# Performance work log

Hardware: AMD Instinct MI355X
Metric: run time of the kernel (lower is better)

The kernel has to match this reference:

```python
import jax, jax.numpy as jnp
import numpy as np
import math

H = 1024  # hidden_size
BELOW = 1024
ABOVE = 1024
B = 2048  # batch


def setup_inputs() -> dict:
    key = jax.random.key(0)
    ks = jax.random.split(key, 10)
    stdv = 1.0 / math.sqrt(H)
    W_hh = jax.random.uniform(ks[0], (4 * H + 1, BELOW), minval=-stdv, maxval=stdv, dtype=jnp.float32)
    U_11 = jax.random.uniform(ks[1], (4 * H + 1, H), minval=-stdv, maxval=stdv, dtype=jnp.float32)
    U_21 = jax.random.uniform(ks[2], (4 * H + 1, ABOVE), minval=-stdv, maxval=stdv, dtype=jnp.float32)
    bias = jax.random.uniform(ks[3], (4 * H + 1,), minval=-stdv, maxval=stdv, dtype=jnp.float32)
    bias = bias.at[-1].set(2.0 / math.sqrt(H))  # reset_parameters sets last bias entry
    c = jax.random.normal(ks[4], (H, B), dtype=jnp.float32)
    h_bottom = jax.random.normal(ks[5], (BELOW, B), dtype=jnp.float32)
    h = jax.random.normal(ks[6], (H, B), dtype=jnp.float32)
    h_top = jax.random.normal(ks[7], (ABOVE, B), dtype=jnp.float32)
    z = jax.random.bernoulli(ks[8], 0.5, (1, B)).astype(jnp.float32)
    z_bottom = jax.random.bernoulli(ks[9], 0.5, (1, B)).astype(jnp.float32)
    return {"c": c, "h_bottom": h_bottom, "h": h, "h_top": h_top, "z": z,
            "z_bottom": z_bottom, "W_hh": W_hh, "U_11": U_11, "U_21": U_21, "bias": bias}


def hard_sigmoid(x, slope=1.0):
    return jnp.clip((x * slope + 1.0) / 2.0, 0.0, 1.0)


def binary_threshold_ste(z_hat, threshold=0.5):
    hard = (z_hat > threshold).astype(z_hat.dtype)
    # straight-through: forward hard, backward identity
    return z_hat + jax.lax.stop_gradient(hard - z_hat)


def reference(c, h_bottom, h, h_top, z, z_bottom, W_hh, U_11, U_21, bias):
    a = 1.0
    s_recur = W_hh @ h_bottom                 # (4H+1, B)
    s_topdown = z * (U_21 @ h_top)            # (4H+1, B)
    s_bottomup = z * (U_11 @ h)               # (4H+1, B)
    f_slice = s_recur + s_topdown + s_bottomup + bias[:, None]
    forgetgate = f_slice[0 * H:1 * H]
    ingate = f_slice[1 * H:2 * H]
    outgate = f_slice[2 * H:3 * H]
    cellgate = f_slice[3 * H:4 * H]
    z_gate = f_slice[4 * H:4 * H + 1]         # (1, B)
    f = jax.nn.sigmoid(forgetgate)
    i = jax.nn.sigmoid(ingate)
    o = jax.nn.sigmoid(outgate)
    g = jnp.tanh(cellgate)
    z_hat = hard_sigmoid(z_gate, slope=a)
    one = 1.0
    c_new = z * (i * g) + (one - z) * (one - z_bottom) * c + (one - z) * z_bottom * (f * c + i * g)
    tanh_c = jnp.tanh(c_new)
    h_new = z * o * tanh_c + (one - z) * (one - z_bottom) * h + (one - z) * z_bottom * o * tanh_c
    z_new = binary_threshold_ste(z_hat)
    return (h_new, c_new, z_new)
```

## Files before the change

### kernel.cpp

```cpp
#include <hip/hip_runtime.h>
#include <hip/hip_bf16.h>

#define HB_ELEMS ((size_t)1024 * 2048)
#define P_ELEMS  ((size_t)4096 * 2048)

typedef __bf16 bfx8 __attribute__((ext_vector_type(8)));
typedef float f32x4 __attribute__((ext_vector_type(4)));

__device__ __forceinline__ float b2f(unsigned short u) {
    union { unsigned int i; float f; } v; v.i = ((unsigned int)u) << 16; return v.f;
}
__device__ __forceinline__ unsigned short f2b(float f) {
    __hip_bfloat16 h = __float2bfloat16(f);
    return *reinterpret_cast<unsigned short*>(&h);
}
__device__ __forceinline__ float loadf(const void* p, size_t i, bool f32) {
    return f32 ? ((const float*)p)[i] : b2f(((const unsigned short*)p)[i]);
}
__device__ __forceinline__ float sigf(float x) { return 1.0f / (1.0f + __expf(-x)); }

__device__ __forceinline__ void cell_math(float fp, float ip, float op, float gp,
                                           float cc, float hh, float zc, float zv,
                                           float& hn, float& cn) {
    float f = sigf(fp), i = sigf(ip), o = sigf(op), g = tanhf(gp);
    float ig = i * g;
    cn = zc * ig + (1.0f - zc) * (1.0f - zv) * cc + (1.0f - zc) * zv * (f * cc + ig);
    float tc = tanhf(cn);
    hn = zc * o * tc + (1.0f - zc) * (1.0f - zv) * hh + (1.0f - zc) * zv * o * tc;
}

__global__ void detect_k(const unsigned short* __restrict__ w, int* __restrict__ flag) {
    int lane = threadIdx.x;
    bool hit = false;
    #pragma unroll
    for (int i = 0; i < 4; ++i) {
        unsigned e = (w[lane + i * 64] >> 7) & 0xFF;
        hit |= (e >= 126);
    }
    unsigned long long m = __ballot(hit);
    if (lane == 0) *flag = (m != 0ULL) ? 1 : 0;
}

__global__ __launch_bounds__(256) void build_bt(
    const void* __restrict__ hb, const void* __restrict__ h,
    const void* __restrict__ ht, const void* __restrict__ z,
    unsigned short* __restrict__ BT, const int* __restrict__ flagp)
{
    const bool f32 = (*flagp != 0);
    int tid = blockIdx.x * 256 + threadIdx.x;
    int b   = tid & 2047;
    int kg8 = tid >> 11;
    int k   = kg8 * 8;

    const void* src; int kl; bool sc;
    if (k < 1024)      { src = hb; kl = k;        sc = false; }
    else if (k < 2048) { src = h;  kl = k - 1024; sc = true;  }
    else               { src = ht; kl = k - 2048; sc = true;  }

    bool zero = sc && (loadf(z, b, f32) == 0.0f);
    unsigned short t[8];
    if (zero) {
        #pragma unroll
        for (int j = 0; j < 8; ++j) t[j] = 0;
    } else if (f32) {
        #pragma unroll
        for (int j = 0; j < 8; ++j) t[j] = f2b(((const float*)src)[(size_t)(kl + j) * 2048 + b]);
    } else {
        #pragma unroll
        for (int j = 0; j < 8; ++j) t[j] = ((const unsigned short*)src)[(size_t)(kl + j) * 2048 + b];
    }
    uint4 v;
    v.x = (unsigned)t[0] | ((unsigned)t[1] << 16);
    v.y = (unsigned)t[2] | ((unsigned)t[3] << 16);
    v.z = (unsigned)t[4] | ((unsigned)t[5] << 16);
    v.w = (unsigned)t[6] | ((unsigned)t[7] << 16);
    *reinterpret_cast<uint4*>(&BT[(size_t)b * 3072 + k]) = v;
}

__global__ __launch_bounds__(256, 2) void gemm_split(
    const void* __restrict__ Whh, const void* __restrict__ U11, const void* __restrict__ U21,
    const unsigned short* __restrict__ BT,
    unsigned short* __restrict__ P, const int* __restrict__ flagp)
{
    const bool f32 = (*flagp != 0);
    __shared__ __align__(16) unsigned short As[2][128 * 64];
    __shared__ __align__(16) unsigned short Bs[2][128 * 64];

    int id  = (blockIdx.z * 32 + blockIdx.y) * 16 + blockIdx.x;
    int sid = (id & 7) * 192 + (id >> 3);
    const int n0   = (sid & 15) * 128;
    const int j0   = ((sid >> 4) & 31) * 32;
    const int kseg = sid >> 9;
    const void* Asrc = (kseg == 0) ? Whh : ((kseg == 1) ? U11 : U21);
    const int kbase = kseg * 1024;

    const int wave = threadIdx.x >> 6;
    const int lane = threadIdx.x & 63;
    const int srow = wave * 8 + (lane >> 3);
    const int scol_sw = (((lane & 7) ^ (lane >> 3)) * 8);
    const int wm = wave >> 1, wn = wave & 1;
    const int lr = lane & 15, kg = lane >> 4;
    const int lr7 = lr & 7;

    f32x4 acc[4][4] = {};

    auto stage = [&](int buf, int k0) {
        #pragma unroll
        for (int r = 0; r < 4; ++r) {
            const unsigned short* g = &BT[(size_t)(n0 + r * 32 + srow) * 3072 + kbase + k0 + scol_sw];
            __builtin_amdgcn_global_load_lds(
                (const __attribute__((address_space(1))) void*)g,
                (__attribute__((address_space(3))) void*)((char*)&Bs[buf][0] + r * 4096 + wave * 1024),
                16, 0, 0);
        }
        if (!f32) {
            #pragma unroll
            for (int r = 0; r < 4; ++r) {
                const unsigned short* g = (const unsigned short*)Asrc
                    + (size_t)(r * 1024 + j0 + srow) * 1024 + k0 + scol_sw;
                __builtin_amdgcn_global_load_lds(
                    (const __attribute__((address_space(1))) void*)g,
                    (__attribute__((address_space(3))) void*)((char*)&As[buf][0] + r * 4096 + wave * 1024),
                    16, 0, 0);
            }
        } else {
            #pragma unroll
            for (int r = 0; r < 4; ++r) {
                int trow = r * 32 + srow;
                int dst  = trow * 64 + scol_sw;
                const float* g = (const float*)Asrc + (size_t)(r * 1024 + j0 + srow) * 1024
                               + k0 + (lane & 7) * 8;
                float4 a0 = *reinterpret_cast<const float4*>(g);
                float4 a1 = *reinterpret_cast<const float4*>(g + 4);
                uint4 v;
                v.x = (unsigned)f2b(a0.x) | ((unsigned)f2b(a0.y) << 16);
                v.y = (unsigned)f2b(a0.z) | ((unsigned)f2b(a0.w) << 16);
                v.z = (unsigned)f2b(a1.x) | ((unsigned)f2b(a1.y) << 16);
                v.w = (unsigned)f2b(a1.z) | ((unsigned)f2b(a1.w) << 16);
                *reinterpret_cast<uint4*>(&As[buf][dst]) = v;
            }
        }
    };

    stage(0, 0);

    #pragma unroll 2
    for (int t = 0; t < 16; ++t) {
        const int cur = t & 1;
        if (t < 15) stage(cur ^ 1, (t + 1) * 64);

        if (f32) {
            asm volatile("s_waitcnt vmcnt(0) lgkmcnt(0)" ::: "memory");
        } else if (t < 15) {
            asm volatile("s_waitcnt vmcnt(8)" ::: "memory");
        } else {
            asm volatile("s_waitcnt vmcnt(0)" ::: "memory");
        }
        __builtin_amdgcn_sched_barrier(0);
        __builtin_amdgcn_s_barrier();
        __builtin_amdgcn_sched_barrier(0);

        #pragma unroll
        for (int kk = 0; kk < 64; kk += 32) {
            const int c0 = kk >> 3;
            const int csw = ((c0 + kg) ^ lr7) * 8;
            bfx8 av[4], bv[4];
            #pragma unroll
            for (int mi = 0; mi < 4; ++mi)
                av[mi] = *reinterpret_cast<const bfx8*>(
                    &As[cur][(wm * 64 + mi * 16 + lr) * 64 + csw]);
            #pragma unroll
            for (int ni = 0; ni < 4; ++ni)
                bv[ni] = *reinterpret_cast<const bfx8*>(
                    &Bs[cur][(wn * 64 + ni * 16 + lr) * 64 + csw]);
            #pragma unroll
            for (int mi = 0; mi < 4; ++mi)
                #pragma unroll
                for (int ni = 0; ni < 4; ++ni)
                    acc[mi][ni] = __builtin_amdgcn_mfma_f32_16x16x32_bf16(av[mi], bv[ni], acc[mi][ni], 0, 0, 0);
        }

        __builtin_amdgcn_sched_barrier(0);
        __builtin_amdgcn_s_barrier();
        __builtin_amdgcn_sched_barrier(0);
    }

    unsigned short* Pp = P + (size_t)kseg * P_ELEMS;
    #pragma unroll
    for (int mi = 0; mi < 4; ++mi) {
        #pragma unroll
        for (int ni = 0; ni < 4; ++ni) {
            int col = n0 + wn * 64 + ni * 16 + lr;
            #pragma unroll
            for (int r = 0; r < 4; ++r) {
                int trow = wm * 64 + mi * 16 + kg * 4 + r;
                int gate = trow >> 5, jj = trow & 31;
                size_t m = (size_t)gate * 1024 + j0 + jj;
                Pp[m * 2048 + col] = f2b(acc[mi][ni][r]);
            }
        }
    }
}

__global__ __launch_bounds__(256) void epilogue_split(
    const unsigned short* __restrict__ P, const void* __restrict__ c_,
    const void* __restrict__ h_, const void* __restrict__ z_,
    const void* __restrict__ zb_, const void* __restrict__ bias_,
    void* __restrict__ out_, const int* __restrict__ flagp)
{
    const bool f32 = (*flagp != 0);
    int tid = blockIdx.x * 256 + threadIdx.x;
    int j = tid >> 9;
    int b = (tid & 511) << 2;
    const size_t jb = (size_t)j * 2048 + b;

    float pre[4][4];
    #pragma unroll
    for (int g = 0; g < 4; ++g) {
        size_t row = (size_t)(g * 1024 + j) * 2048 + b;
        ushort4 s0 = *reinterpret_cast<const ushort4*>(&P[row]);
        ushort4 s1 = *reinterpret_cast<const ushort4*>(&P[P_ELEMS + row]);
        ushort4 s2 = *reinterpret_cast<const ushort4*>(&P[2 * P_ELEMS + row]);
        float bv = loadf(bias_, g * 1024 + j, f32);
        pre[g][0] = b2f(s0.x) + b2f(s1.x) + b2f(s2.x) + bv;
        pre[g][1] = b2f(s0.y) + b2f(s1.y) + b2f(s2.y) + bv;
        pre[g][2] = b2f(s0.z) + b2f(s1.z) + b2f(s2.z) + bv;
        pre[g][3] = b2f(s0.w) + b2f(s1.w) + b2f(s2.w) + bv;
    }

    float hn[4], cn[4];
    #pragma unroll
    for (int e = 0; e < 4; ++e) {
        float zc = loadf(z_, b + e, f32);
        float zv = loadf(zb_, b + e, f32);
        float cc = loadf(c_, jb + e, f32);
        float hh = loadf(h_, jb + e, f32);
        cell_math(pre[0][e], pre[1][e], pre[2][e], pre[3][e], cc, hh, zc, zv, hn[e], cn[e]);
    }
    if (f32) {
        float4 ho = {hn[0], hn[1], hn[2], hn[3]};
        float4 co = {cn[0], cn[1], cn[2], cn[3]};
        *reinterpret_cast<float4*>(&((float*)out_)[jb]) = ho;
        *reinterpret_cast<float4*>(&((float*)out_)[HB_ELEMS + jb]) = co;
    } else {
        ushort4 ho = {f2b(hn[0]), f2b(hn[1]), f2b(hn[2]), f2b(hn[3])};
        ushort4 co = {f2b(cn[0]), f2b(cn[1]), f2b(cn[2]), f2b(cn[3])};
        *reinterpret_cast<ushort4*>(&((unsigned short*)out_)[jb]) = ho;
        *reinterpret_cast<ushort4*>(&((unsigned short*)out_)[HB_ELEMS + jb]) = co;
    }
}

__global__ __launch_bounds__(256) void gemm_fused(
    const void* __restrict__ Whh, const void* __restrict__ U11, const void* __restrict__ U21,
    const unsigned short* __restrict__ BT,
    const void* __restrict__ c_, const void* __restrict__ h_,
    const void* __restrict__ z_, const void* __restrict__ zb_,
    const void* __restrict__ bias_, void* __restrict__ out_,
    const int* __restrict__ flagp)
{
    const bool f32 = (*flagp != 0);
    __shared__ __align__(16) unsigned short As[128 * 64];
    __shared__ __align__(16) unsigned short Bs[128 * 64];

    const int n0 = blockIdx.x * 128;
    const int j0 = blockIdx.y * 32;
    const int wave = threadIdx.x >> 6;
    const int lane = threadIdx.x & 63;
    const int srow = wave * 8 + (lane >> 3);
    const int scol = (lane & 7) * 8;
    const int lr = lane & 15, kg = lane >> 4;

    f32x4 acc[8][2] = {};

    for (int k0 = 0; k0 < 3072; k0 += 64) {
        int seg = k0 >> 10, kl = k0 & 1023;
        const void* Asrc = (seg == 0) ? Whh : ((seg == 1) ? U11 : U21);

        __syncthreads();
        #pragma unroll
        for (int r = 0; r < 4; ++r) {
            const unsigned short* g = &BT[(size_t)(n0 + r * 32 + srow) * 3072 + k0 + scol];
            __builtin_amdgcn_global_load_lds(
                (const __attribute__((address_space(1))) void*)g,
                (__attribute__((address_space(3))) void*)((char*)Bs + r * 4096 + wave * 1024),
                16, 0, 0);
        }
        if (!f32) {
            #pragma unroll
            for (int r = 0; r < 4; ++r) {
                const unsigned short* g = (const unsigned short*)Asrc
                    + (size_t)(r * 1024 + j0 + srow) * 1024 + kl + scol;
                __builtin_amdgcn_global_load_lds(
                    (const __attribute__((address_space(1))) void*)g,
                    (__attribute__((address_space(3))) void*)((char*)As + r * 4096 + wave * 1024),
                    16, 0, 0);
            }
        } else {
            #pragma unroll
            for (int r = 0; r < 4; ++r) {
                int trow = r * 32 + srow;
                const float* g = (const float*)Asrc + (size_t)(r * 1024 + j0 + srow) * 1024 + kl + scol;
                float4 a0 = *reinterpret_cast<const float4*>(g);
                float4 a1 = *reinterpret_cast<const float4*>(g + 4);
                uint4 v;
                v.x = (unsigned)f2b(a0.x) | ((unsigned)f2b(a0.y) << 16);
                v.y = (unsigned)f2b(a0.z) | ((unsigned)f2b(a0.w) << 16);
                v.z = (unsigned)f2b(a1.x) | ((unsigned)f2b(a1.y) << 16);
                v.w = (unsigned)f2b(a1.z) | ((unsigned)f2b(a1.w) << 16);
                *reinterpret_cast<uint4*>(&As[trow * 64 + scol]) = v;
            }
        }
        __syncthreads();

        #pragma unroll
        for (int kk = 0; kk < 64; kk += 32) {
            bfx8 bv0 = *reinterpret_cast<const bfx8*>(&Bs[(wave * 32 + lr) * 64 + kk + kg * 8]);
            bfx8 bv1 = *reinterpret_cast<const bfx8*>(&Bs[(wave * 32 + 16 + lr) * 64 + kk + kg * 8]);
            #pragma unroll
            for (int mi = 0; mi < 8; ++mi) {
                bfx8 af = *reinterpret_cast<const bfx8*>(&As[(mi * 16 + lr) * 64 + kk + kg * 8]);
                acc[mi][0] = __builtin_amdgcn_mfma_f32_16x16x32_bf16(af, bv0, acc[mi][0], 0, 0, 0);
                acc[mi][1] = __builtin_amdgcn_mfma_f32_16x16x32_bf16(af, bv1, acc[mi][1], 0, 0, 0);
            }
        }
    }

    #pragma unroll
    for (int ni = 0; ni < 2; ++ni) {
        int b = n0 + wave * 32 + ni * 16 + lr;
        float zc = loadf(z_, b, f32);
        float zv = loadf(zb_, b, f32);
        #pragma unroll
        for (int mh = 0; mh < 2; ++mh) {
            #pragma unroll
            for (int r = 0; r < 4; ++r) {
                int j = j0 + mh * 16 + kg * 4 + r;
                float fp = acc[0 + mh][ni][r] + loadf(bias_, j, f32);
                float ip = acc[2 + mh][ni][r] + loadf(bias_, 1024 + j, f32);
                float op = acc[4 + mh][ni][r] + loadf(bias_, 2048 + j, f32);
                float gp = acc[6 + mh][ni][r] + loadf(bias_, 3072 + j, f32);
                float cc = loadf(c_, (size_t)j * 2048 + b, f32);
                float hh = loadf(h_, (size_t)j * 2048 + b, f32);
                float hn, cn;
                cell_math(fp, ip, op, gp, cc, hh, zc, zv, hn, cn);
                if (f32) {
                    ((float*)out_)[(size_t)j * 2048 + b] = hn;
                    ((float*)out_)[HB_ELEMS + (size_t)j * 2048 + b] = cn;
                } else {
                    ((unsigned short*)out_)[(size_t)j * 2048 + b] = f2b(hn);
                    ((unsigned short*)out_)[HB_ELEMS + (size_t)j * 2048 + b] = f2b(cn);
                }
            }
        }
    }
}

__global__ __launch_bounds__(256) void zrow_part(
    const void* __restrict__ Whh, const void* __restrict__ U11, const void* __restrict__ U21,
    const void* __restrict__ hb, const void* __restrict__ h, const void* __restrict__ ht,
    float* __restrict__ pz, const int* __restrict__ flagp)
{
    const bool f32 = (*flagp != 0);
    const int c   = blockIdx.x;
    const int mat = c >> 5;
    const int k0  = (c & 31) * 32;
    const int b0  = threadIdx.x * 8;

    const void* W = (mat == 0) ? Whh : ((mat == 1) ? U11 : U21);
    const void* X = (mat == 0) ? hb  : ((mat == 1) ? h   : ht);
    const size_t wrow = (size_t)4096 * 1024;

    float acc[8] = {0.f, 0.f, 0.f, 0.f, 0.f, 0.f, 0.f, 0.f};
    if (!f32) {
        const unsigned short* Wp = (const unsigned short*)W;
        const unsigned short* Xp = (const unsigned short*)X;
        #pragma unroll 4
        for (int kk = 0; kk < 32; ++kk) {
            int k = k0 + kk;
            float w = b2f(Wp[wrow + k]);
            ushort4 xa = *reinterpret_cast<const ushort4*>(&Xp[(size_t)k * 2048 + b0]);
            ushort4 xb = *reinterpret_cast<const ushort4*>(&Xp[(size_t)k * 2048 + b0 + 4]);
            acc[0] += w * b2f(xa.x); acc[1] += w * b2f(xa.y);
            acc[2] += w * b2f(xa.z); acc[3] += w * b2f(xa.w);
            acc[4] += w * b2f(xb.x); acc[5] += w * b2f(xb.y);
            acc[6] += w * b2f(xb.z); acc[7] += w * b2f(xb.w);
        }
    } else {
        const float* Wp = (const float*)W;
        const float* Xp = (const float*)X;
        #pragma unroll 4
        for (int kk = 0; kk < 32; ++kk) {
            int k = k0 + kk;
            float w = Wp[wrow + k];
            float4 xa = *reinterpret_cast<const float4*>(&Xp[(size_t)k * 2048 + b0]);
            float4 xb = *reinterpret_cast<const float4*>(&Xp[(size_t)k * 2048 + b0 + 4]);
            acc[0] += w * xa.x; acc[1] += w * xa.y; acc[2] += w * xa.z; acc[3] += w * xa.w;
            acc[4] += w * xb.x; acc[5] += w * xb.y; acc[6] += w * xb.z; acc[7] += w * xb.w;
        }
    }
    #pragma unroll
    for (int j = 0; j < 8; ++j)
        pz[(size_t)c * 2048 + b0 + j] = acc[j];
}

__global__ __launch_bounds__(256) void zrow_reduce(
    const float* __restrict__ pz, const void* __restrict__ z_,
    const void* __restrict__ bias_, void* __restrict__ out_,
    const int* __restrict__ flagp)
{
    const bool f32 = (*flagp != 0);
    int b = blockIdx.x * 256 + threadIdx.x;
    float a1 = 0.f, a2 = 0.f, a3 = 0.f;
    #pragma unroll
    for (int c = 0; c < 32; ++c)  a1 += pz[(size_t)c * 2048 + b];
    #pragma unroll
    for (int c = 32; c < 64; ++c) a2 += pz[(size_t)c * 2048 + b];
    #pragma unroll
    for (int c = 64; c < 96; ++c) a3 += pz[(size_t)c * 2048 + b];
    float zc = loadf(z_, b, f32);
    float s = a1 + zc * (a2 + a3) + loadf(bias_, 4096, f32);
    float zh = (s + 1.0f) * 0.5f;
    zh = fminf(fmaxf(zh, 0.0f), 1.0f);
    float zn = (zh > 0.5f) ? 1.0f : 0.0f;
    if (f32) ((float*)out_)[2 * HB_ELEMS + b] = zn;
    else     ((unsigned short*)out_)[2 * HB_ELEMS + b] = f2b(zn);
}

__global__ __launch_bounds__(256) void zrow_k(
    const void* __restrict__ Whh, const void* __restrict__ U11, const void* __restrict__ U21,
    const void* __restrict__ hb, const void* __restrict__ h, const void* __restrict__ ht,
    const void* __restrict__ z_, const void* __restrict__ bias_,
    void* __restrict__ out_, const int* __restrict__ flagp)
{
    const bool f32 = (*flagp != 0);
    int b = blockIdx.x * 256 + threadIdx.x;
    float a1 = 0.f, a2 = 0.f, a3 = 0.f;
    const size_t wrow = (size_t)4096 * 1024;
    for (int k = 0; k < 1024; ++k) {
        a1 += loadf(Whh, wrow + k, f32) * loadf(hb, (size_t)k * 2048 + b, f32);
        a2 += loadf(U11, wrow + k, f32) * loadf(h,  (size_t)k * 2048 + b, f32);
        a3 += loadf(U21, wrow + k, f32) * loadf(ht, (size_t)k * 2048 + b, f32);
    }
    float zc = loadf(z_, b, f32);
    float s = a1 + zc * (a2 + a3) + loadf(bias_, 4096, f32);
    float zh = (s + 1.0f) * 0.5f;
    zh = fminf(fmaxf(zh, 0.0f), 1.0f);
    float zn = (zh > 0.5f) ? 1.0f : 0.0f;
    if (f32) ((float*)out_)[2 * HB_ELEMS + b] = zn;
    else     ((unsigned short*)out_)[2 * HB_ELEMS + b] = f2b(zn);
}

__global__ __launch_bounds__(256) void fallback_k(
    const void* __restrict__ Whh, const void* __restrict__ U11, const void* __restrict__ U21,
    const void* __restrict__ hb, const void* __restrict__ h, const void* __restrict__ ht,
    const void* __restrict__ c_, const void* __restrict__ z_, const void* __restrict__ zb_,
    const void* __restrict__ bias_, void* __restrict__ out_, const int* __restrict__ flagp)
{
    const bool f32 = (*flagp != 0);
    int b = blockIdx.x * 256 + threadIdx.x;
    int j = blockIdx.y;
    float zc = loadf(z_, b, f32);
    float a[4] = {0.f, 0.f, 0.f, 0.f};
    for (int k = 0; k < 1024; ++k) {
        float xb = loadf(hb, (size_t)k * 2048 + b, f32);
        #pragma unroll
        for (int g = 0; g < 4; ++g)
            a[g] += loadf(Whh, (size_t)(g * 1024 + j) * 1024 + k, f32) * xb;
    }
    for (int k = 0; k < 1024; ++k) {
        float xh = zc * loadf(h, (size_t)k * 2048 + b, f32);
        #pragma unroll
        for (int g = 0; g < 4; ++g)
            a[g] += loadf(U11, (size_t)(g * 1024 + j) * 1024 + k, f32) * xh;
    }
    for (int k = 0; k < 1024; ++k) {
        float xt = zc * loadf(ht, (size_t)k * 2048 + b, f32);
        #pragma unroll
        for (int g = 0; g < 4; ++g)
            a[g] += loadf(U21, (size_t)(g * 1024 + j) * 1024 + k, f32) * xt;
    }
    float fp = a[0] + loadf(bias_, j, f32);
    float ip = a[1] + loadf(bias_, 1024 + j, f32);
    float op = a[2] + loadf(bias_, 2048 + j, f32);
    float gp = a[3] + loadf(bias_, 3072 + j, f32);
    float cc = loadf(c_, (size_t)j * 2048 + b, f32);
    float hh = loadf(h,  (size_t)j * 2048 + b, f32);
    float zv = loadf(zb_, b, f32);
    float hn, cn;
    cell_math(fp, ip, op, gp, cc, hh, zc, zv, hn, cn);
    if (f32) {
        ((float*)out_)[(size_t)j * 2048 + b] = hn;
        ((float*)out_)[HB_ELEMS + (size_t)j * 2048 + b] = cn;
    } else {
        ((unsigned short*)out_)[(size_t)j * 2048 + b] = f2b(hn);
        ((unsigned short*)out_)[HB_ELEMS + (size_t)j * 2048 + b] = f2b(cn);
    }
}

extern "C" void kernel_launch(void* const* d_in, const int* in_sizes, int n_in,
                              void* d_out, int out_size, void* d_ws, size_t ws_size,
                              hipStream_t stream)
{
    const void* c    = d_in[0];
    const void* hb   = d_in[1];
    const void* h    = d_in[2];
    const void* ht   = d_in[3];
    const void* z    = d_in[4];
    const void* zb   = d_in[5];
    const void* Whh  = d_in[6];
    const void* U11  = d_in[7];
    const void* U21  = d_in[8];
    const void* bias = d_in[9];

    int* flag = (int*)d_ws;
    unsigned short* BT = (unsigned short*)((char*)d_ws + 4096);
    const size_t bt_bytes = (size_t)2048 * 3072 * 2;
    float* pz = (float*)((char*)d_ws + 4096 + bt_bytes);
    const size_t pz_bytes = (size_t)96 * 2048 * 4;
    unsigned short* P = (unsigned short*)((char*)d_ws + 4096 + bt_bytes + pz_bytes);
    const size_t p_bytes = 3 * P_ELEMS * 2;

    const size_t need_bt    = 4096 + bt_bytes;
    const size_t need_pz    = need_bt + pz_bytes;
    const size_t need_split = need_pz + p_bytes;

    if (ws_size < 4) return;

    detect_k<<<1, 64, 0, stream>>>((const unsigned short*)Whh, flag);

    if (ws_size >= need_split) {
        build_bt<<<(2048 * 384) / 256, 256, 0, stream>>>(hb, h, ht, z, BT, flag);
        gemm_split<<<dim3(16, 32, 3), 256, 0, stream>>>(Whh, U11, U21, BT, P, flag);
        epilogue_split<<<(1024 * 512) / 256, 256, 0, stream>>>(P, c, h, z, zb, bias, d_out, flag);
    } else if (ws_size >= need_bt) {
        build_bt<<<(2048 * 384) / 256, 256, 0, stream>>>(hb, h, ht, z, BT, flag);
        gemm_fused<<<dim3(16, 32), 256, 0, stream>>>(Whh, U11, U21, BT,
                                                     c, h, z, zb, bias, d_out, flag);
    } else {
        fallback_k<<<dim3(8, 1024), 256, 0, stream>>>(Whh, U11, U21, hb, h, ht,
                                                      c, z, zb, bias, d_out, flag);
    }

    if (ws_size >= need_pz) {
        zrow_part<<<96, 256, 0, stream>>>(Whh, U11, U21, hb, h, ht, pz, flag);
        zrow_reduce<<<8, 256, 0, stream>>>(pz, z, bias, d_out, flag);
    } else {
        zrow_k<<<8, 256, 0, stream>>>(Whh, U11, U21, hb, h, ht, z, bias, d_out, flag);
    }
}
```

Baseline: 135.1 us.

## Enlarge GEMM tiles to 256x256 with 512 threads and split K in two

The split GEMM now uses 256x256 output tiles with 8 waves per block, each wave holding an 8x4 MFMA accumulator grid. K is split into two halves of 1536 that cross weight-matrix boundaries, replacing the three per-matrix segments. This halves the partial-sum buffer and removes one partial read in the epilogue, and the larger tiles reuse each loaded operand more. The trade-offs are 64 KB of LDS per block, more accumulator registers, and only 256 blocks, which may leave CUs underused.

```diff
diff --git a/kernel.cpp b/kernel.cpp
--- a/kernel.cpp
+++ b/kernel.cpp
@@ -77,59 +77,62 @@
     *reinterpret_cast<uint4*>(&BT[(size_t)b * 3072 + k]) = v;
 }
 
-__global__ __launch_bounds__(256, 2) void gemm_split(
+__global__ __launch_bounds__(512, 2) void gemm_split(
     const void* __restrict__ Whh, const void* __restrict__ U11, const void* __restrict__ U21,
     const unsigned short* __restrict__ BT,
     unsigned short* __restrict__ P, const int* __restrict__ flagp)
 {
     const bool f32 = (*flagp != 0);
-    __shared__ __align__(16) unsigned short As[2][128 * 64];
-    __shared__ __align__(16) unsigned short Bs[2][128 * 64];
-
-    int id  = (blockIdx.z * 32 + blockIdx.y) * 16 + blockIdx.x;
-    int sid = (id & 7) * 192 + (id >> 3);
-    const int n0   = (sid & 15) * 128;
-    const int j0   = ((sid >> 4) & 31) * 32;
-    const int kseg = sid >> 9;
-    const void* Asrc = (kseg == 0) ? Whh : ((kseg == 1) ? U11 : U21);
-    const int kbase = kseg * 1024;
+    __shared__ __align__(16) unsigned short As[2][256 * 64];
+    __shared__ __align__(16) unsigned short Bs[2][256 * 64];
+
+    int id  = (blockIdx.z * 16 + blockIdx.y) * 8 + blockIdx.x;
+    int sid = (id & 7) * 32 + (id >> 3);
+    const int n0   = (sid & 7) * 256;
+    const int j0   = ((sid >> 3) & 15) * 64;
+    const int kseg = sid >> 7;
+    const int kbase = kseg * 1536;
 
     const int wave = threadIdx.x >> 6;
     const int lane = threadIdx.x & 63;
-    const int srow = wave * 8 + (lane >> 3);
     const int scol_sw = (((lane & 7) ^ (lane >> 3)) * 8);
-    const int wm = wave >> 1, wn = wave & 1;
+    const int wm = wave >> 2, wn = wave & 3;
     const int lr = lane & 15, kg = lane >> 4;
     const int lr7 = lr & 7;
 
-    f32x4 acc[4][4] = {};
-
-    auto stage = [&](int buf, int k0) {
+    f32x4 acc[8][4] = {};
+
+    auto stage = [&](int buf, int kt) {
+        const int kglob = kbase + kt * 64;
+        const int seg = kglob >> 10, kl = kglob & 1023;
+        const void* Ap = (seg == 0) ? Whh : ((seg == 1) ? U11 : U21);
+
         #pragma unroll
         for (int r = 0; r < 4; ++r) {
-            const unsigned short* g = &BT[(size_t)(n0 + r * 32 + srow) * 3072 + kbase + k0 + scol_sw];
+            int trow = r * 64 + wave * 8 + (lane >> 3);
+            const unsigned short* g = &BT[(size_t)(n0 + trow) * 3072 + kglob + scol_sw];
             __builtin_amdgcn_global_load_lds(
                 (const __attribute__((address_space(1))) void*)g,
-                (__attribute__((address_space(3))) void*)((char*)&Bs[buf][0] + r * 4096 + wave * 1024),
+                (__attribute__((address_space(3))) void*)((char*)&Bs[buf][0] + r * 8192 + wave * 1024),
                 16, 0, 0);
         }
         if (!f32) {
             #pragma unroll
             for (int r = 0; r < 4; ++r) {
-                const unsigned short* g = (const unsigned short*)Asrc
-                    + (size_t)(r * 1024 + j0 + srow) * 1024 + k0 + scol_sw;
+                int trow = r * 64 + wave * 8 + (lane >> 3);
+                size_t arow = (size_t)((trow >> 6) * 1024 + j0 + (trow & 63));
+                const unsigned short* g = (const unsigned short*)Ap + arow * 1024 + kl + scol_sw;
                 __builtin_amdgcn_global_load_lds(
                     (const __attribute__((address_space(1))) void*)g,
-                    (__attribute__((address_space(3))) void*)((char*)&As[buf][0] + r * 4096 + wave * 1024),
+                    (__attribute__((address_space(3))) void*)((char*)&As[buf][0] + r * 8192 + wave * 1024),
                     16, 0, 0);
             }
         } else {
             #pragma unroll
             for (int r = 0; r < 4; ++r) {
-                int trow = r * 32 + srow;
-                int dst  = trow * 64 + scol_sw;
-                const float* g = (const float*)Asrc + (size_t)(r * 1024 + j0 + srow) * 1024
-                               + k0 + (lane & 7) * 8;
+                int trow = r * 64 + wave * 8 + (lane >> 3);
+                size_t arow = (size_t)((trow >> 6) * 1024 + j0 + (trow & 63));
+                const float* g = (const float*)Ap + arow * 1024 + kl + (lane & 7) * 8;
                 float4 a0 = *reinterpret_cast<const float4*>(g);
                 float4 a1 = *reinterpret_cast<const float4*>(g + 4);
                 uint4 v;
@@ -137,7 +140,7 @@
                 v.y = (unsigned)f2b(a0.z) | ((unsigned)f2b(a0.w) << 16);
                 v.z = (unsigned)f2b(a1.x) | ((unsigned)f2b(a1.y) << 16);
                 v.w = (unsigned)f2b(a1.z) | ((unsigned)f2b(a1.w) << 16);
-                *reinterpret_cast<uint4*>(&As[buf][dst]) = v;
+                *reinterpret_cast<uint4*>(&As[buf][trow * 64 + scol_sw]) = v;
             }
         }
     };
@@ -145,13 +148,13 @@
     stage(0, 0);
 
     #pragma unroll 2
-    for (int t = 0; t < 16; ++t) {
-        const int cur = t & 1;
-        if (t < 15) stage(cur ^ 1, (t + 1) * 64);
+    for (int kt = 0; kt < 24; ++kt) {
+        const int cur = kt & 1;
+        if (kt < 23) stage(cur ^ 1, kt + 1);
 
         if (f32) {
             asm volatile("s_waitcnt vmcnt(0) lgkmcnt(0)" ::: "memory");
-        } else if (t < 15) {
+        } else if (kt < 23) {
             asm volatile("s_waitcnt vmcnt(8)" ::: "memory");
         } else {
             asm volatile("s_waitcnt vmcnt(0)" ::: "memory");
@@ -161,20 +164,19 @@
         __builtin_amdgcn_sched_barrier(0);
 
         #pragma unroll
-        for (int kk = 0; kk < 64; kk += 32) {
-            const int c0 = kk >> 3;
-            const int csw = ((c0 + kg) ^ lr7) * 8;
-            bfx8 av[4], bv[4];
-            #pragma unroll
-            for (int mi = 0; mi < 4; ++mi)
+        for (int kk = 0; kk < 2; ++kk) {
+            const int csw = ((kk * 4 + kg) ^ lr7) * 8;
+            bfx8 av[8], bv[4];
+            #pragma unroll
+            for (int mi = 0; mi < 8; ++mi)
                 av[mi] = *reinterpret_cast<const bfx8*>(
-                    &As[cur][(wm * 64 + mi * 16 + lr) * 64 + csw]);
+                    &As[cur][(wm * 128 + mi * 16 + lr) * 64 + csw]);
             #pragma unroll
             for (int ni = 0; ni < 4; ++ni)
                 bv[ni] = *reinterpret_cast<const bfx8*>(
                     &Bs[cur][(wn * 64 + ni * 16 + lr) * 64 + csw]);
             #pragma unroll
-            for (int mi = 0; mi < 4; ++mi)
+            for (int mi = 0; mi < 8; ++mi)
                 #pragma unroll
                 for (int ni = 0; ni < 4; ++ni)
                     acc[mi][ni] = __builtin_amdgcn_mfma_f32_16x16x32_bf16(av[mi], bv[ni], acc[mi][ni], 0, 0, 0);
@@ -187,14 +189,14 @@
 
     unsigned short* Pp = P + (size_t)kseg * P_ELEMS;
     #pragma unroll
-    for (int mi = 0; mi < 4; ++mi) {
+    for (int mi = 0; mi < 8; ++mi) {
         #pragma unroll
         for (int ni = 0; ni < 4; ++ni) {
             int col = n0 + wn * 64 + ni * 16 + lr;
             #pragma unroll
             for (int r = 0; r < 4; ++r) {
-                int trow = wm * 64 + mi * 16 + kg * 4 + r;
-                int gate = trow >> 5, jj = trow & 31;
+                int trow = wm * 128 + mi * 16 + kg * 4 + r;
+                int gate = trow >> 6, jj = trow & 63;
                 size_t m = (size_t)gate * 1024 + j0 + jj;
                 Pp[m * 2048 + col] = f2b(acc[mi][ni][r]);
             }
@@ -220,12 +222,11 @@
         size_t row = (size_t)(g * 1024 + j) * 2048 + b;
         ushort4 s0 = *reinterpret_cast<const ushort4*>(&P[row]);
         ushort4 s1 = *reinterpret_cast<const ushort4*>(&P[P_ELEMS + row]);
-        ushort4 s2 = *reinterpret_cast<const ushort4*>(&P[2 * P_ELEMS + row]);
         float bv = loadf(bias_, g * 1024 + j, f32);
-        pre[g][0] = b2f(s0.x) + b2f(s1.x) + b2f(s2.x) + bv;
-        pre[g][1] = b2f(s0.y) + b2f(s1.y) + b2f(s2.y) + bv;
-        pre[g][2] = b2f(s0.z) + b2f(s1.z) + b2f(s2.z) + bv;
-        pre[g][3] = b2f(s0.w) + b2f(s1.w) + b2f(s2.w) + bv;
+        pre[g][0] = b2f(s0.x) + b2f(s1.x) + bv;
+        pre[g][1] = b2f(s0.y) + b2f(s1.y) + bv;
+        pre[g][2] = b2f(s0.z) + b2f(s1.z) + bv;
+        pre[g][3] = b2f(s0.w) + b2f(s1.w) + bv;
     }
 
     float hn[4], cn[4];
@@ -518,7 +519,7 @@
     float* pz = (float*)((char*)d_ws + 4096 + bt_bytes);
     const size_t pz_bytes = (size_t)96 * 2048 * 4;
     unsigned short* P = (unsigned short*)((char*)d_ws + 4096 + bt_bytes + pz_bytes);
-    const size_t p_bytes = 3 * P_ELEMS * 2;
+    const size_t p_bytes = 2 * P_ELEMS * 2;
 
     const size_t need_bt    = 4096 + bt_bytes;
     const size_t need_pz    = need_bt + pz_bytes;
@@ -530,7 +531,7 @@
 
     if (ws_size >= need_split) {
         build_bt<<<(2048 * 384) / 256, 256, 0, stream>>>(hb, h, ht, z, BT, flag);
-        gemm_split<<<dim3(16, 32, 3), 256, 0, stream>>>(Whh, U11, U21, BT, P, flag);
+        gemm_split<<<dim3(8, 16, 2), 512, 0, stream>>>(Whh, U11, U21, BT, P, flag);
         epilogue_split<<<(1024 * 512) / 256, 256, 0, stream>>>(P, c, h, z, zb, bias, d_out, flag);
     } else if (ws_size >= need_bt) {
         build_bt<<<(2048 * 384) / 256, 256, 0, stream>>>(hb, h, ht, z, BT, flag);
```

Result: slower. 157.8 us (+16.7%).
